# Kernel optimization log

Hardware: AMD Instinct MI355X
Metric: run time of the kernel (lower is better)

## Reference

```python
import jax, jax.numpy as jnp
import numpy as np

N_NODE = 40000
EMB = 100
LAYERS = 2
B = 512
L = 50
N = 50
E = 800000


def _l2norm(x, axis=-1, eps=1e-12):
    n = jnp.sqrt(jnp.sum(x * x, axis=axis, keepdims=True))
    return x / jnp.maximum(n, eps)


def _item_conv(rows, cols, vals, emb, b):
    # sparse A @ X repeated LAYERS times, stack, l2-normalize rows, weighted sum
    finals = [emb]
    x = emb
    for _ in range(LAYERS):
        x = jax.ops.segment_sum(vals[:, None] * x[cols], rows, num_segments=emb.shape[0])
        finals.append(x)
    f = _l2norm(jnp.stack(finals, 0))                      # [LAYERS+1, n, d]
    return jnp.sum(b[:, None, None] * f, axis=0)


def _session_conv(adj_dense, emb, a):
    finals = [emb]
    x = emb
    for _ in range(LAYERS):
        x = adj_dense @ x
        finals.append(x)
    f = _l2norm(jnp.stack(finals, 0))
    return jnp.sum(a[:, None, None] * f, axis=0)


def _gat(h, adj, a0, a1, a2, a3):
    # e_k[b,i,j] = leakyrelu(sum_d h[b,i,d]*h[b,j,d]*a_k[d]); never materialize [B,N,N,D]
    def score(a):
        return jax.nn.leaky_relu(jnp.einsum('bid,bjd->bij', h * a[:, 0], h), 0.2)
    e0, e1, e2, e3 = score(a0), score(a1), score(a2), score(a3)
    neg = jnp.float32(-9e15)
    alpha = jnp.where(adj == 1, e0, neg)
    alpha = jnp.where(adj == 2, e1, alpha)
    alpha = jnp.where(adj == 3, e2, alpha)
    alpha = jnp.where(adj == 4, e3, alpha)
    alpha = jax.nn.softmax(alpha, axis=-1)
    return jnp.einsum('bij,bjd->bid', alpha, h)


def _get_seq(emb_table, rev, h, alias, mix=0.8):
    seq_h = emb_table[rev]                                  # [B,L,D]
    bidx = jnp.arange(rev.shape[0])[:, None]
    seq_h_ = h[bidx, alias]                                 # [B,L,D]
    return (1.0 - mix) * seq_h + mix * seq_h_               # eval: dropout = identity


def _soft_attention(seq_h, mask_f, session_len, pos_emb, w1_W, w1_b, glu1_W, glu1_b, glu2_W, w2):
    hs = jnp.sum(seq_h, axis=1) / session_len               # [B,D]
    pos = jnp.broadcast_to(pos_emb[:seq_h.shape[1]][None], seq_h.shape)
    nh = jnp.tanh(jnp.concatenate([pos, seq_h], -1) @ w1_W.T + w1_b)
    nh = jax.nn.sigmoid(nh @ glu1_W.T + glu1_b + (hs @ glu2_W.T)[:, None, :])
    beta = (nh @ w2) * mask_f[..., None]                    # [B,L,1]
    return jnp.sum(beta * seq_h, axis=1)                    # [B,D]


def setup_inputs() -> dict:
    key = jax.random.key(0)
    ks = jax.random.split(key, 30)
    stdv = 1.0 / np.sqrt(EMB)
    u = lambda k, s: jax.random.uniform(k, s, jnp.float32, -stdv, stdv)
    return {
        'tar': jax.random.randint(ks[0], (B,), 0, N_NODE),
        'reversed_sess_item': jax.random.randint(ks[1], (B, L), 0, N_NODE + 1),
        'mask': jnp.ones((B, L), jnp.int32),
        'session_len': jnp.ones((B, 1), jnp.float32),
        'session_adj': jax.random.uniform(ks[2], (B, B), jnp.float32),
        'is_train': 0,
        'items': jax.random.randint(ks[3], (B, N), 0, N_NODE + 1),
        'adj': jax.random.randint(ks[4], (B, N, N), 0, 5),
        'alias_session': jax.random.randint(ks[5], (B, L), 0, N),
        'gnn_rows': jax.random.randint(ks[6], (E,), 0, N_NODE),
        'gnn_cols': jax.random.randint(ks[7], (E,), 0, N_NODE),
        'gnn_vals': jax.random.uniform(ks[8], (E,), jnp.float32),
        'nodes_emb': u(ks[9], (N_NODE, EMB)),
        'b_item': jnp.ones((LAYERS + 1,), jnp.float32),
        'a_sess': jnp.ones((LAYERS + 1,), jnp.float32),
        'a0': u(ks[10], (EMB, 1)), 'a1': u(ks[11], (EMB, 1)),
        'a2': u(ks[12], (EMB, 1)), 'a3': u(ks[13], (EMB, 1)),
        'w1_W': u(ks[14], (EMB, 2 * EMB)), 'w1_b': u(ks[15], (EMB,)),
        'w2': u(ks[16], (EMB, 1)),
        'glu1_W': u(ks[17], (EMB, EMB)), 'glu1_b': u(ks[18], (EMB,)),
        'glu2_W': u(ks[19], (EMB, EMB)),
        'pos_emb': u(ks[20], (150, EMB)),
    }


def reference(tar, reversed_sess_item, mask, session_len, session_adj, is_train,
              items, adj, alias_session, gnn_rows, gnn_cols, gnn_vals,
              nodes_emb, b_item, a_sess, a0, a1, a2, a3,
              w1_W, w1_b, w2, glu1_W, glu1_b, glu2_W, pos_emb):
    mask_f = mask.astype(jnp.float32)
    zeros = jnp.zeros((1, EMB), jnp.float32)
    emb_gnn = _item_conv(gnn_rows, gnn_cols, gnn_vals, nodes_emb, b_item)
    # eval mode: both dropouts are identity
    e1t = jnp.concatenate([zeros, emb_gnn], 0)
    e2t = jnp.concatenate([zeros, emb_gnn], 0)
    embeddings = e1t + e2t

    h1 = _gat(e1t[items], adj, a0, a1, a2, a3)
    h1 = _get_seq(e1t, reversed_sess_item, h1, alias_session, 0.8)
    h2 = _gat(e2t[items], adj, a0, a1, a2, a3)
    h2 = _get_seq(e2t, reversed_sess_item, h2, alias_session, 0.8)

    sel1 = _soft_attention(h1, mask_f, session_len, pos_emb, w1_W, w1_b, glu1_W, glu1_b, glu2_W, w2)
    sel1 = _session_conv(session_adj, sel1, a_sess)
    sel2 = _soft_attention(h2, mask_f, session_len, pos_emb, w1_W, w1_b, glu1_W, glu1_b, glu2_W, w2)
    sel2 = _session_conv(session_adj, sel2, a_sess)

    con_loss = jnp.float32(0.0)  # is_train == 0 (inference path)

    seq_h = sel1 + sel2
    scores = seq_h @ embeddings[1:].T                       # [B, N_NODE]
    logp = jax.nn.log_softmax(scores + 1e-8, axis=-1)
    loss = -jnp.mean(logp[jnp.arange(scores.shape[0]), tar])
    return (con_loss, loss, scores)
```

## Files before the change

kernel.cpp:

```cpp
#include <hip/hip_runtime.h>
#include <hip/hip_bf16.h>
#include <math.h>

#define N_NODE 40000
#define EMB 100
#define BB 512
#define LL 50
#define NI 50
#define EDG 800000
#define SCAN_BLOCKS 157

typedef short s16x8 __attribute__((ext_vector_type(8)));
typedef float f32x4 __attribute__((ext_vector_type(4)));

__global__ void khist(const int* __restrict__ rows, int* __restrict__ counts) {
  int e = blockIdx.x * 256 + threadIdx.x;
  atomicAdd(&counts[rows[e]], 1);
}

__global__ __launch_bounds__(256) void kscan1(const int* __restrict__ counts,
                                              int* __restrict__ scanout,
                                              int* __restrict__ blocksums, int n) {
  __shared__ int wsum[4];
  int tid = threadIdx.x;
  int i = blockIdx.x * 256 + tid;
  int v = (i < n) ? counts[i] : 0;
  int x = v;
  #pragma unroll
  for (int off = 1; off < 64; off <<= 1) {
    int t = __shfl_up(x, off, 64);
    if ((tid & 63) >= off) x += t;
  }
  int w = tid >> 6, lane = tid & 63;
  if (lane == 63) wsum[w] = x;
  __syncthreads();
  int woff = 0;
  #pragma unroll
  for (int k = 0; k < 4; ++k) woff += (k < w) ? wsum[k] : 0;
  int incl = x + woff;
  if (i < n) scanout[i] = incl - v;
  if (tid == 255) blocksums[blockIdx.x] = incl;
}

__global__ __launch_bounds__(256) void kscan2(int* __restrict__ blocksums, int nb) {
  __shared__ int wsum[4];
  int tid = threadIdx.x;
  int v = (tid < nb) ? blocksums[tid] : 0;
  int x = v;
  #pragma unroll
  for (int off = 1; off < 64; off <<= 1) {
    int t = __shfl_up(x, off, 64);
    if ((tid & 63) >= off) x += t;
  }
  int w = tid >> 6, lane = tid & 63;
  if (lane == 63) wsum[w] = x;
  __syncthreads();
  int woff = 0;
  #pragma unroll
  for (int k = 0; k < 4; ++k) woff += (k < w) ? wsum[k] : 0;
  if (tid < nb) blocksums[tid] = x + woff - v;
}

__global__ __launch_bounds__(256) void kscan3(const int* __restrict__ scanout,
                                              const int* __restrict__ blocksums,
                                              int* __restrict__ starts,
                                              int* __restrict__ cursor, int n) {
  int i = blockIdx.x * 256 + threadIdx.x;
  if (i < n) {
    int s = scanout[i] + blocksums[blockIdx.x];
    starts[i] = s;
    cursor[i] = s;
  }
}

__global__ void kfill(const int* __restrict__ rows, const int* __restrict__ cols,
                      const float* __restrict__ vals, int* __restrict__ cursor,
                      int* __restrict__ colS, float* __restrict__ valS) {
  int e = blockIdx.x * 256 + threadIdx.x;
  int r = rows[e];
  int p = atomicAdd(&cursor[r], 1);
  colS[p] = cols[e];
  valS[p] = vals[e];
}

__global__ __launch_bounds__(256) void kspmm(const int* __restrict__ starts,
                                             const int* __restrict__ counts,
                                             const int* __restrict__ colS,
                                             const float* __restrict__ valS,
                                             const float* __restrict__ x,
                                             float* __restrict__ out) {
  int row = blockIdx.x * 4 + (threadIdx.x >> 6);
  int lane = threadIdx.x & 63;
  int s = starts[row], cnt = counts[row];
  bool act = lane < 50;
  int d2 = (act ? lane : 49) * 2;
  float ax = 0.f, ay = 0.f;
  for (int base = 0; base < cnt; base += 64) {
    int nb = cnt - base; if (nb > 64) nb = 64;
    int cl = 0; float vl = 0.f;
    if (lane < nb) {
      cl = colS[s + base + lane];
      vl = valS[s + base + lane];
    }
    int t = 0;
    for (; t + 4 <= nb; t += 4) {
      int c0 = __shfl(cl, t),     c1 = __shfl(cl, t + 1);
      int c2 = __shfl(cl, t + 2), c3 = __shfl(cl, t + 3);
      float v0 = __shfl(vl, t),     v1 = __shfl(vl, t + 1);
      float v2 = __shfl(vl, t + 2), v3 = __shfl(vl, t + 3);
      float2 g0 = *(const float2*)(x + (size_t)c0 * EMB + d2);
      float2 g1 = *(const float2*)(x + (size_t)c1 * EMB + d2);
      float2 g2 = *(const float2*)(x + (size_t)c2 * EMB + d2);
      float2 g3 = *(const float2*)(x + (size_t)c3 * EMB + d2);
      ax += v0 * g0.x; ay += v0 * g0.y;
      ax += v1 * g1.x; ay += v1 * g1.y;
      ax += v2 * g2.x; ay += v2 * g2.y;
      ax += v3 * g3.x; ay += v3 * g3.y;
    }
    for (; t < nb; ++t) {
      int c = __shfl(cl, t);
      float v = __shfl(vl, t);
      float2 g = *(const float2*)(x + (size_t)c * EMB + d2);
      ax += v * g.x; ay += v * g.y;
    }
  }
  if (act) {
    float2 o; o.x = ax; o.y = ay;
    *(float2*)(out + (size_t)row * EMB + d2) = o;
  }
}

__global__ void kcomb(const float* __restrict__ x0, const float* __restrict__ x1,
                      const float* __restrict__ x2, const float* __restrict__ bI,
                      float* __restrict__ emb) {
  int n = blockIdx.x * 4 + (threadIdx.x >> 6);
  int lane = threadIdx.x & 63;
  int d0 = lane, d1 = lane + 64;
  bool h1 = d1 < EMB;
  size_t base = (size_t)n * EMB;
  float v00 = x0[base + d0], v01 = h1 ? x0[base + d1] : 0.f;
  float v10 = x1[base + d0], v11 = h1 ? x1[base + d1] : 0.f;
  float v20 = x2[base + d0], v21 = h1 ? x2[base + d1] : 0.f;
  float q0 = v00 * v00 + v01 * v01;
  float q1 = v10 * v10 + v11 * v11;
  float q2 = v20 * v20 + v21 * v21;
  #pragma unroll
  for (int off = 32; off; off >>= 1) {
    q0 += __shfl_xor(q0, off);
    q1 += __shfl_xor(q1, off);
    q2 += __shfl_xor(q2, off);
  }
  float r0 = 1.f / fmaxf(sqrtf(q0), 1e-12f);
  float r1 = 1.f / fmaxf(sqrtf(q1), 1e-12f);
  float r2 = 1.f / fmaxf(sqrtf(q2), 1e-12f);
  float b0 = bI[0], b1 = bI[1], b2 = bI[2];
  emb[base + d0] = b0 * v00 * r0 + b1 * v10 * r1 + b2 * v20 * r2;
  if (h1) emb[base + d1] = b0 * v01 * r0 + b1 * v11 * r1 + b2 * v21 * r2;
}

__global__ __launch_bounds__(256) void kgat(
    const float* __restrict__ emb, const int* __restrict__ items,
    const int* __restrict__ adj,
    const float* __restrict__ a0p, const float* __restrict__ a1p,
    const float* __restrict__ a2p, const float* __restrict__ a3p,
    float* __restrict__ hgat) {
  __shared__ __align__(16) float hl[64 * 108];
  __shared__ __align__(16) float as[4 * 100];
  __shared__ float al[4][4][64];
  int b = blockIdx.x, half = blockIdx.y;
  int tid = threadIdx.x;
  for (int idx = tid; idx < 400; idx += 256) {
    int k = idx / 100, d = idx % 100;
    const float* ap = (k == 0) ? a0p : (k == 1) ? a1p : (k == 2) ? a2p : a3p;
    as[idx] = ap[d];
  }
  for (int idx = tid; idx < 64 * 50; idx += 256) {
    int i = idx / 50, d2 = (idx % 50) * 2;
    float2 v; v.x = 0.f; v.y = 0.f;
    if (i < NI) {
      int node = items[b * NI + i];
      if (node != 0) v = *(const float2*)(emb + (size_t)(node - 1) * EMB + d2);
    }
    *(float2*)&hl[i * 108 + d2] = v;
  }
  __syncthreads();
  int w = tid >> 6, lane = tid & 63;
  int i0 = half * 25 + w * 7;
  int nIw = 25 - w * 7; if (nIw > 7) nIw = 7;
  const float* hjrow = &hl[lane * 108];
  int u2 = lane >> 5, dq = lane & 31;
  int dqc = (dq < 25) ? dq : 24;
  for (int g = 0; g < nIw; g += 4) {
    int ib = i0 + g;
    int rem = nIw - g;
    int ir[4], av[4];
    const float* asel[4];
    #pragma unroll
    for (int u = 0; u < 4; ++u) {
      int i = ib + u; ir[u] = (i < NI) ? i : NI - 1;
      av[u] = (lane < NI) ? adj[(size_t)b * (NI * NI) + ir[u] * NI + lane] : 0;
      int k = av[u] - 1; if (k < 0) k = 0; if (k > 3) k = 3;
      asel[u] = &as[k * 100];
    }
    float acc[4];
    #pragma unroll
    for (int u = 0; u < 4; ++u) acc[u] = 0.f;
    for (int d0 = 0; d0 < 100; d0 += 4) {
      float4 hj = *(const float4*)(hjrow + d0);
      #pragma unroll
      for (int u = 0; u < 4; ++u) {
        float4 hi = *(const float4*)&hl[ir[u] * 108 + d0];
        float4 aw = *(const float4*)(asel[u] + d0);
        float p0 = hi.x * hj.x, p1 = hi.y * hj.y;
        float p2 = hi.z * hj.z, p3 = hi.w * hj.w;
        acc[u] += p0 * aw.x + p1 * aw.y + p2 * aw.z + p3 * aw.w;
      }
    }
    #pragma unroll
    for (int u = 0; u < 4; ++u) {
      float sv = acc[u];
      sv = (sv >= 0.f) ? sv : 0.2f * sv;
      float e = (av[u] == 0) ? -9e15f : sv;
      if (lane >= NI) e = -INFINITY;
      float m = e;
      #pragma unroll
      for (int off = 32; off; off >>= 1) m = fmaxf(m, __shfl_xor(m, off));
      float p = expf(e - m);
      float s = p;
      #pragma unroll
      for (int off = 32; off; off >>= 1) s += __shfl_xor(s, off);
      al[w][u][lane] = p / s;
    }
    #pragma unroll
    for (int pass = 0; pass < 2; ++pass) {
      int u = pass * 2 + u2;
      int i = ib + u;
      const float* alr = al[w][u];
      float ox = 0.f, oy = 0.f, oz = 0.f, ow = 0.f;
      for (int j = 0; j < NI; ++j) {
        float a = alr[j];
        float4 hv = *(const float4*)&hl[j * 108 + dqc * 4];
        ox += a * hv.x; oy += a * hv.y; oz += a * hv.z; ow += a * hv.w;
      }
      if (dq < 25 && u < rem) {
        float4 o4; o4.x = ox; o4.y = oy; o4.z = oz; o4.w = ow;
        *(float4*)&hgat[((size_t)b * NI + i) * EMB + dq * 4] = o4;
      }
    }
  }
}

__global__ void kseq(const float* __restrict__ emb, const int* __restrict__ rev,
                     const int* __restrict__ alias, const float* __restrict__ hgat,
                     float* __restrict__ hseq) {
  int idx = blockIdx.x * 256 + threadIdx.x;
  int b = idx / 5000, r = idx % 5000, l = r / 100, d = r % 100;
  int node = rev[b * LL + l];
  float sh = (node == 0) ? 0.f : emb[(size_t)(node - 1) * EMB + d];
  int a = alias[b * LL + l];
  float shh = hgat[((size_t)b * NI + a) * EMB + d];
  hseq[idx] = 0.2f * sh + 0.8f * shh;
}

__global__ void kprep_t(const float* __restrict__ w1W, const float* __restrict__ g1W,
                        const float* __restrict__ g2W, float* __restrict__ w1t2,
                        float* __restrict__ g1t, float* __restrict__ g2t) {
  int idx = blockIdx.x * 256 + threadIdx.x;
  if (idx >= 10000) return;
  int c = idx / 100, o = idx % 100;
  w1t2[c * 100 + o] = w1W[o * 200 + 100 + c];
  g1t[c * 100 + o] = g1W[o * 100 + c];
  g2t[c * 100 + o] = g2W[o * 100 + c];
}

__global__ void kprep_pos(const float* __restrict__ posE, const float* __restrict__ w1W,
                          const float* __restrict__ w1b, float* __restrict__ posW) {
  int idx = blockIdx.x * 256 + threadIdx.x;
  if (idx >= 5000) return;
  int l = idx / 100, o = idx % 100;
  float acc = w1b[o];
  for (int c = 0; c < 100; ++c) acc += posE[l * 100 + c] * w1W[o * 200 + c];
  posW[idx] = acc;
}

__global__ __launch_bounds__(256) void ksoft(
    const float* __restrict__ hseqG, const float* __restrict__ slenp,
    const int* __restrict__ maskp,
    const float* __restrict__ posW, const float* __restrict__ w1t2,
    const float* __restrict__ glu1t, const float* __restrict__ glu1b,
    const float* __restrict__ glu2t, const float* __restrict__ w2,
    float* __restrict__ sel) {
  __shared__ float hq[LL * 101];
  __shared__ float nh[LL * 100];
  __shared__ float red[25 * 52];
  __shared__ float hs_s[100];
  __shared__ float g_s[100];
  __shared__ float beta_s[LL];
  int b = blockIdx.x, tid = threadIdx.x;
  for (int idx = tid; idx < LL * 100; idx += 256) {
    int l = idx / 100, d = idx % 100;
    hq[l * 101 + d] = hseqG[((size_t)b * LL + l) * 100 + d];
  }
  __syncthreads();
  if (tid < 100) {
    float s = 0.f;
    for (int l = 0; l < LL; ++l) s += hq[l * 101 + tid];
    hs_s[tid] = s / slenp[b];
  }
  __syncthreads();
  if (tid < 100) {
    float acc = 0.f;
    for (int c = 0; c < 100; ++c) acc += hs_s[c] * glu2t[c * 100 + tid];
    g_s[tid] = acc;
  }
  int lg = tid / 25, og = tid % 25;
  if (tid < 250) {
    float acc[5][4];
    #pragma unroll
    for (int j = 0; j < 5; ++j) {
      float4 p = *(const float4*)&posW[(lg * 5 + j) * 100 + og * 4];
      acc[j][0] = p.x; acc[j][1] = p.y; acc[j][2] = p.z; acc[j][3] = p.w;
    }
    for (int c = 0; c < 100; ++c) {
      float4 wv = *(const float4*)&w1t2[c * 100 + og * 4];
      float hv[5];
      #pragma unroll
      for (int j = 0; j < 5; ++j) hv[j] = hq[(lg * 5 + j) * 101 + c];
      #pragma unroll
      for (int j = 0; j < 5; ++j) {
        acc[j][0] += hv[j] * wv.x;
        acc[j][1] += hv[j] * wv.y;
        acc[j][2] += hv[j] * wv.z;
        acc[j][3] += hv[j] * wv.w;
      }
    }
    #pragma unroll
    for (int j = 0; j < 5; ++j) {
      float4 t;
      t.x = tanhf(acc[j][0]); t.y = tanhf(acc[j][1]);
      t.z = tanhf(acc[j][2]); t.w = tanhf(acc[j][3]);
      *(float4*)&nh[(lg * 5 + j) * 100 + og * 4] = t;
    }
  }
  __syncthreads();
  if (tid < 250) {
    float4 gb = *(const float4*)&glu1b[og * 4];
    float4 gg = *(const float4*)&g_s[og * 4];
    float base0 = gg.x + gb.x, base1 = gg.y + gb.y, base2 = gg.z + gb.z, base3 = gg.w + gb.w;
    float acc[5][4];
    #pragma unroll
    for (int j = 0; j < 5; ++j) {
      acc[j][0] = base0; acc[j][1] = base1; acc[j][2] = base2; acc[j][3] = base3;
    }
    for (int c = 0; c < 100; ++c) {
      float4 wv = *(const float4*)&glu1t[c * 100 + og * 4];
      float hv[5];
      #pragma unroll
      for (int j = 0; j < 5; ++j) hv[j] = nh[(lg * 5 + j) * 100 + c];
      #pragma unroll
      for (int j = 0; j < 5; ++j) {
        acc[j][0] += hv[j] * wv.x;
        acc[j][1] += hv[j] * wv.y;
        acc[j][2] += hv[j] * wv.z;
        acc[j][3] += hv[j] * wv.w;
      }
    }
    float4 w2v = *(const float4*)&w2[og * 4];
    #pragma unroll
    for (int j = 0; j < 5; ++j) {
      float s0 = w2v.x / (1.f + expf(-acc[j][0]));
      float s1 = w2v.y / (1.f + expf(-acc[j][1]));
      float s2 = w2v.z / (1.f + expf(-acc[j][2]));
      float s3 = w2v.w / (1.f + expf(-acc[j][3]));
      red[og * 52 + lg * 5 + j] = (s0 + s1) + (s2 + s3);
    }
  }
  __syncthreads();
  if (tid < LL) {
    float s = 0.f;
    for (int og2 = 0; og2 < 25; ++og2) s += red[og2 * 52 + tid];
    beta_s[tid] = s * (float)maskp[b * LL + tid];
  }
  __syncthreads();
  if (tid < 100) {
    float acc = 0.f;
    for (int l = 0; l < LL; ++l) acc += beta_s[l] * hq[l * 101 + tid];
    sel[(size_t)b * 100 + tid] = acc;
  }
}

__global__ void ksess(const float* __restrict__ adjS, const float* __restrict__ x,
                      float* __restrict__ out) {
  int b = blockIdx.x, d = threadIdx.x;
  if (d >= 100) return;
  const float* ar = adjS + (size_t)b * BB;
  float a0 = 0.f, a1 = 0.f, a2 = 0.f, a3 = 0.f;
  for (int j = 0; j < BB; j += 4) {
    a0 += ar[j]     * x[(j)     * 100 + d];
    a1 += ar[j + 1] * x[(j + 1) * 100 + d];
    a2 += ar[j + 2] * x[(j + 2) * 100 + d];
    a3 += ar[j + 3] * x[(j + 3) * 100 + d];
  }
  out[(size_t)b * 100 + d] = (a0 + a1) + (a2 + a3);
}

__global__ void ksesscomb(const float* __restrict__ x0, const float* __restrict__ x1,
                          const float* __restrict__ x2, const float* __restrict__ aS,
                          float* __restrict__ out) {
  int b = blockIdx.x * 4 + (threadIdx.x >> 6);
  int lane = threadIdx.x & 63;
  int d0 = lane, d1 = lane + 64;
  bool h1 = d1 < EMB;
  size_t base = (size_t)b * EMB;
  float v00 = x0[base + d0], v01 = h1 ? x0[base + d1] : 0.f;
  float v10 = x1[base + d0], v11 = h1 ? x1[base + d1] : 0.f;
  float v20 = x2[base + d0], v21 = h1 ? x2[base + d1] : 0.f;
  float q0 = v00 * v00 + v01 * v01;
  float q1 = v10 * v10 + v11 * v11;
  float q2 = v20 * v20 + v21 * v21;
  #pragma unroll
  for (int off = 32; off; off >>= 1) {
    q0 += __shfl_xor(q0, off);
    q1 += __shfl_xor(q1, off);
    q2 += __shfl_xor(q2, off);
  }
  float r0 = 1.f / fmaxf(sqrtf(q0), 1e-12f);
  float r1 = 1.f / fmaxf(sqrtf(q1), 1e-12f);
  float r2 = 1.f / fmaxf(sqrtf(q2), 1e-12f);
  float b0 = aS[0], b1 = aS[1], b2 = aS[2];
  out[base + d0] = 2.f * (b0 * v00 * r0 + b1 * v10 * r1 + b2 * v20 * r2);
  if (h1) out[base + d1] = 2.f * (b0 * v01 * r0 + b1 * v11 * r1 + b2 * v21 * r2);
}

__global__ void kprepB(const float* __restrict__ emb, unsigned short* __restrict__ bHi,
                       unsigned short* __restrict__ bLo) {
  int idx = blockIdx.x * 256 + threadIdx.x;
  int n = idx >> 7, k = idx & 127;
  float v = (k < EMB) ? 2.f * emb[(size_t)n * EMB + k] : 0.f;
  __hip_bfloat16 h = __float2bfloat16(v);
  float rem = v - __bfloat162float(h);
  __hip_bfloat16 l = __float2bfloat16(rem);
  bHi[idx] = *reinterpret_cast<unsigned short*>(&h);
  bLo[idx] = *reinterpret_cast<unsigned short*>(&l);
}

__global__ void kprepA(const float* __restrict__ seqh, unsigned short* __restrict__ aHi,
                       unsigned short* __restrict__ aLo) {
  int idx = blockIdx.x * 256 + threadIdx.x;
  int n = idx >> 7, k = idx & 127;
  float v = (k < EMB) ? seqh[(size_t)n * EMB + k] : 0.f;
  __hip_bfloat16 h = __float2bfloat16(v);
  float rem = v - __bfloat162float(h);
  __hip_bfloat16 l = __float2bfloat16(rem);
  aHi[idx] = *reinterpret_cast<unsigned short*>(&h);
  aLo[idx] = *reinterpret_cast<unsigned short*>(&l);
}

__global__ __launch_bounds__(256) void kscoresM(
    const unsigned short* __restrict__ aHi, const unsigned short* __restrict__ aLo,
    const unsigned short* __restrict__ bHi, const unsigned short* __restrict__ bLo,
    float* __restrict__ outS) {
  __shared__ __align__(16) unsigned short Bh[64 * 136];
  __shared__ __align__(16) unsigned short Bl[64 * 136];
  int tid = threadIdx.x;
  int n0 = blockIdx.x * 64, b0 = blockIdx.y * 64;
  int w = tid >> 6, lane = tid & 63;
  int ln = lane & 15, quad = lane >> 4;

  const unsigned short* aRowH = aHi + (size_t)(b0 + w * 16 + ln) * 128 + quad * 8;
  const unsigned short* aRowL = aLo + (size_t)(b0 + w * 16 + ln) * 128 + quad * 8;
  s16x8 ah[4], al[4];
  #pragma unroll
  for (int s = 0; s < 4; ++s) {
    ah[s] = *(const s16x8*)(aRowH + s * 32);
    al[s] = *(const s16x8*)(aRowL + s * 32);
  }

  #pragma unroll
  for (int it = 0; it < 4; ++it) {
    int seg = tid + it * 256;
    int r = seg >> 4, q = seg & 15;
    *(s16x8*)&Bh[r * 136 + q * 8] = *(const s16x8*)&bHi[(size_t)(n0 + r) * 128 + q * 8];
    *(s16x8*)&Bl[r * 136 + q * 8] = *(const s16x8*)&bLo[(size_t)(n0 + r) * 128 + q * 8];
  }
  __syncthreads();

  f32x4 acc[4];
  #pragma unroll
  for (int t = 0; t < 4; ++t) acc[t] = (f32x4){0.f, 0.f, 0.f, 0.f};

  #pragma unroll
  for (int s = 0; s < 4; ++s) {
    #pragma unroll
    for (int t = 0; t < 4; ++t) {
      s16x8 bh = *(const s16x8*)&Bh[(t * 16 + ln) * 136 + s * 32 + quad * 8];
      s16x8 bl = *(const s16x8*)&Bl[(t * 16 + ln) * 136 + s * 32 + quad * 8];
      acc[t] = __builtin_amdgcn_mfma_f32_16x16x32_bf16(ah[s], bh, acc[t], 0, 0, 0);
      acc[t] = __builtin_amdgcn_mfma_f32_16x16x32_bf16(al[s], bh, acc[t], 0, 0, 0);
      acc[t] = __builtin_amdgcn_mfma_f32_16x16x32_bf16(ah[s], bl, acc[t], 0, 0, 0);
    }
  }

  int brow = b0 + w * 16 + quad * 4;
  #pragma unroll
  for (int t = 0; t < 4; ++t) {
    int ncol = n0 + t * 16 + ln;
    #pragma unroll
    for (int r = 0; r < 4; ++r) {
      outS[(size_t)(brow + r) * N_NODE + ncol] = acc[t][r];
    }
  }
}

__global__ __launch_bounds__(256) void klse(const float* __restrict__ outS,
                                            const int* __restrict__ tar,
                                            float* __restrict__ part) {
  __shared__ float ms[256], ss[256];
  int b = blockIdx.x, tid = threadIdx.x;
  const float2* sp = (const float2*)(outS + (size_t)b * N_NODE);
  float m = -INFINITY, s = 0.f;
  for (int i = tid; i < N_NODE / 2; i += 256) {
    float2 v = sp[i];
    float mx = fmaxf(v.x, v.y);
    float add = expf(v.x - mx) + expf(v.y - mx);
    if (mx > m) { s = s * expf(m - mx) + add; m = mx; }
    else s += add * expf(mx - m);
  }
  ms[tid] = m; ss[tid] = s;
  __syncthreads();
  for (int st = 128; st; st >>= 1) {
    if (tid < st) {
      float m2 = ms[tid + st], s2 = ss[tid + st];
      float M = fmaxf(ms[tid], m2);
      ss[tid] = ss[tid] * expf(ms[tid] - M) + s2 * expf(m2 - M);
      ms[tid] = M;
    }
    __syncthreads();
  }
  if (tid == 0) {
    float tsc = outS[(size_t)b * N_NODE + tar[b]];
    part[b] = tsc - (ms[0] + logf(ss[0]));
  }
}

__global__ void kfinal(const float* __restrict__ part, float* __restrict__ out) {
  __shared__ float red[256];
  int tid = threadIdx.x;
  red[tid] = part[tid] + part[tid + 256];
  __syncthreads();
  for (int st = 128; st; st >>= 1) {
    if (tid < st) red[tid] += red[tid + st];
    __syncthreads();
  }
  if (tid == 0) {
    out[0] = 0.f;
    out[1] = -red[0] / (float)BB;
  }
}

extern "C" void kernel_launch(void* const* d_in, const int* in_sizes, int n_in,
                              void* d_out, int out_size, void* d_ws, size_t ws_size,
                              hipStream_t stream) {
  const int* tar    = (const int*)d_in[0];
  const int* rev    = (const int*)d_in[1];
  const int* maskp  = (const int*)d_in[2];
  const float* slen = (const float*)d_in[3];
  const float* sadj = (const float*)d_in[4];
  const int* items  = (const int*)d_in[6];
  const int* adjp   = (const int*)d_in[7];
  const int* alias  = (const int*)d_in[8];
  const int* grows  = (const int*)d_in[9];
  const int* gcols  = (const int*)d_in[10];
  const float* gvals = (const float*)d_in[11];
  const float* nemb = (const float*)d_in[12];
  const float* bI   = (const float*)d_in[13];
  const float* aS   = (const float*)d_in[14];
  const float* a0p  = (const float*)d_in[15];
  const float* a1p  = (const float*)d_in[16];
  const float* a2p  = (const float*)d_in[17];
  const float* a3p  = (const float*)d_in[18];
  const float* w1W  = (const float*)d_in[19];
  const float* w1b  = (const float*)d_in[20];
  const float* w2p  = (const float*)d_in[21];
  const float* g1W  = (const float*)d_in[22];
  const float* g1b  = (const float*)d_in[23];
  const float* g2W  = (const float*)d_in[24];
  const float* posE = (const float*)d_in[25];

  float* W = (float*)d_ws;
  size_t o = 0;
  float* emb_gnn = W + o; o += (size_t)N_NODE * EMB;
  float* x1      = W + o; o += (size_t)N_NODE * EMB;
  float* x2      = W + o; o += (size_t)N_NODE * EMB;
  float* sel     = W + o; o += (size_t)BB * EMB;
  float* y1      = W + o; o += (size_t)BB * EMB;
  float* y2      = W + o; o += (size_t)BB * EMB;
  float* seqh    = W + o; o += (size_t)BB * EMB;
  float* posW    = W + o; o += 5120;
  float* w1t2    = W + o; o += 10000;
  float* glu1t   = W + o; o += 10000;
  float* glu2t   = W + o; o += 10000;
  float* valS    = W + o; o += EDG;
  float* part    = W + o; o += 512;
  int* colS   = (int*)(W + o); o += EDG;
  int* counts = (int*)(W + o); o += N_NODE;
  int* starts = (int*)(W + o); o += N_NODE;
  int* cursor = (int*)(W + o); o += N_NODE;
  int* scantmp = (int*)(W + o); o += N_NODE;
  int* blocksums = (int*)(W + o); o += 256;
  unsigned short* aHi = (unsigned short*)(W + o); o += 32768;
  unsigned short* aLo = (unsigned short*)(W + o); o += 32768;
  float* hgat = x1;
  float* hseq = x2;
  unsigned short* bHi = (unsigned short*)x1;
  unsigned short* bLo = (unsigned short*)x2;

  float* outF = (float*)d_out;
  float* outScores = outF + 2;

  hipMemsetAsync(counts, 0, N_NODE * sizeof(int), stream);
  khist<<<EDG / 256, 256, 0, stream>>>(grows, counts);
  kscan1<<<SCAN_BLOCKS, 256, 0, stream>>>(counts, scantmp, blocksums, N_NODE);
  kscan2<<<1, 256, 0, stream>>>(blocksums, SCAN_BLOCKS);
  kscan3<<<SCAN_BLOCKS, 256, 0, stream>>>(scantmp, blocksums, starts, cursor, N_NODE);
  kfill<<<EDG / 256, 256, 0, stream>>>(grows, gcols, gvals, cursor, colS, valS);
  kspmm<<<N_NODE / 4, 256, 0, stream>>>(starts, counts, colS, valS, nemb, x1);
  kspmm<<<N_NODE / 4, 256, 0, stream>>>(starts, counts, colS, valS, x1, x2);
  kcomb<<<N_NODE / 4, 256, 0, stream>>>(nemb, x1, x2, bI, emb_gnn);
  kgat<<<dim3(BB, 2), 256, 0, stream>>>(emb_gnn, items, adjp, a0p, a1p, a2p, a3p, hgat);
  kseq<<<(BB * LL * EMB) / 256, 256, 0, stream>>>(emb_gnn, rev, alias, hgat, hseq);
  kprep_t<<<40, 256, 0, stream>>>(w1W, g1W, g2W, w1t2, glu1t, glu2t);
  kprep_pos<<<20, 256, 0, stream>>>(posE, w1W, w1b, posW);
  ksoft<<<BB, 256, 0, stream>>>(hseq, slen, maskp, posW, w1t2, glu1t, g1b, glu2t, w2p, sel);
  kprepB<<<(N_NODE * 128) / 256, 256, 0, stream>>>(emb_gnn, bHi, bLo);
  ksess<<<BB, 128, 0, stream>>>(sadj, sel, y1);
  ksess<<<BB, 128, 0, stream>>>(sadj, y1, y2);
  ksesscomb<<<BB / 4, 256, 0, stream>>>(sel, y1, y2, aS, seqh);
  kprepA<<<(BB * 128) / 256, 256, 0, stream>>>(seqh, aHi, aLo);
  kscoresM<<<dim3(N_NODE / 64, BB / 64), 256, 0, stream>>>(aHi, aLo, bHi, bLo, outScores);
  klse<<<BB, 256, 0, stream>>>(outScores, tar, part);
  kfinal<<<1, 256, 0, stream>>>(part, outF);
}
```

Measured before the change: 566.3 us.

## Restructure GAT kernel to one block per session with register-held rows

The GAT kernel now runs one block per session instead of two. Each lane holds its node's embedding row in registers, and the four waves split the neighbour index j into chunks of 13. The softmax max and sum are combined across waves through shared memory, and alpha is written to LDS so the weighted sum can be split by feature quads across waves. The SpMM gather also gains an 8-way unrolled loop to put more loads in flight. The aim is to stop recomputing and re-reading data between the two half-blocks and to raise reuse of the per-row data. The costs are heavy register pressure (25 float4 plus 13 scores per lane), extra block-wide syncs and half as many blocks.

```diff
diff --git a/kernel.cpp b/kernel.cpp
--- a/kernel.cpp
+++ b/kernel.cpp
@@ -103,6 +103,32 @@
       vl = valS[s + base + lane];
     }
     int t = 0;
+    for (; t + 8 <= nb; t += 8) {
+      int c0 = __shfl(cl, t),     c1 = __shfl(cl, t + 1);
+      int c2 = __shfl(cl, t + 2), c3 = __shfl(cl, t + 3);
+      int c4 = __shfl(cl, t + 4), c5 = __shfl(cl, t + 5);
+      int c6 = __shfl(cl, t + 6), c7 = __shfl(cl, t + 7);
+      float v0 = __shfl(vl, t),     v1 = __shfl(vl, t + 1);
+      float v2 = __shfl(vl, t + 2), v3 = __shfl(vl, t + 3);
+      float v4 = __shfl(vl, t + 4), v5 = __shfl(vl, t + 5);
+      float v6 = __shfl(vl, t + 6), v7 = __shfl(vl, t + 7);
+      float2 g0 = *(const float2*)(x + (size_t)c0 * EMB + d2);
+      float2 g1 = *(const float2*)(x + (size_t)c1 * EMB + d2);
+      float2 g2 = *(const float2*)(x + (size_t)c2 * EMB + d2);
+      float2 g3 = *(const float2*)(x + (size_t)c3 * EMB + d2);
+      float2 g4 = *(const float2*)(x + (size_t)c4 * EMB + d2);
+      float2 g5 = *(const float2*)(x + (size_t)c5 * EMB + d2);
+      float2 g6 = *(const float2*)(x + (size_t)c6 * EMB + d2);
+      float2 g7 = *(const float2*)(x + (size_t)c7 * EMB + d2);
+      ax += v0 * g0.x; ay += v0 * g0.y;
+      ax += v1 * g1.x; ay += v1 * g1.y;
+      ax += v2 * g2.x; ay += v2 * g2.y;
+      ax += v3 * g3.x; ay += v3 * g3.y;
+      ax += v4 * g4.x; ay += v4 * g4.y;
+      ax += v5 * g5.x; ay += v5 * g5.y;
+      ax += v6 * g6.x; ay += v6 * g6.y;
+      ax += v7 * g7.x; ay += v7 * g7.y;
+    }
     for (; t + 4 <= nb; t += 4) {
       int c0 = __shfl(cl, t),     c1 = __shfl(cl, t + 1);
       int c2 = __shfl(cl, t + 2), c3 = __shfl(cl, t + 3);
@@ -166,8 +192,9 @@
     float* __restrict__ hgat) {
   __shared__ __align__(16) float hl[64 * 108];
   __shared__ __align__(16) float as[4 * 100];
-  __shared__ float al[4][4][64];
-  int b = blockIdx.x, half = blockIdx.y;
+  __shared__ float alpha_lds[64 * 51];
+  __shared__ float wred[4][2][64];
+  int b = blockIdx.x;
   int tid = threadIdx.x;
   for (int idx = tid; idx < 400; idx += 256) {
     int k = idx / 100, d = idx % 100;
@@ -185,66 +212,88 @@
   }
   __syncthreads();
   int w = tid >> 6, lane = tid & 63;
-  int i0 = half * 25 + w * 7;
-  int nIw = 25 - w * 7; if (nIw > 7) nIw = 7;
-  const float* hjrow = &hl[lane * 108];
-  int u2 = lane >> 5, dq = lane & 31;
-  int dqc = (dq < 25) ? dq : 24;
-  for (int g = 0; g < nIw; g += 4) {
-    int ib = i0 + g;
-    int rem = nIw - g;
-    int ir[4], av[4];
-    const float* asel[4];
-    #pragma unroll
-    for (int u = 0; u < 4; ++u) {
-      int i = ib + u; ir[u] = (i < NI) ? i : NI - 1;
-      av[u] = (lane < NI) ? adj[(size_t)b * (NI * NI) + ir[u] * NI + lane] : 0;
-      int k = av[u] - 1; if (k < 0) k = 0; if (k > 3) k = 3;
-      asel[u] = &as[k * 100];
-    }
-    float acc[4];
-    #pragma unroll
-    for (int u = 0; u < 4; ++u) acc[u] = 0.f;
-    for (int d0 = 0; d0 < 100; d0 += 4) {
-      float4 hj = *(const float4*)(hjrow + d0);
+  int j0 = w * 13;
+  int nj = 50 - j0; if (nj > 13) nj = 13;
+
+  float4 hreg[25];
+  #pragma unroll
+  for (int q = 0; q < 25; ++q) hreg[q] = *(const float4*)&hl[lane * 108 + q * 4];
+
+  int al_lane = (lane < NI) ? lane : NI - 1;
+  const int* adjrow = adj + (size_t)b * (NI * NI) + al_lane * NI + j0;
+  int adjv[13];
+  #pragma unroll
+  for (int t = 0; t < 13; ++t) adjv[t] = (t < nj) ? adjrow[t] : 0;
+
+  float e[13];
+  #pragma unroll
+  for (int jj = 0; jj < 13; ++jj) {
+    float acc = 0.f;
+    if (jj < nj) {
+      int j = j0 + jj;
+      int k = adjv[jj] - 1; k = (k < 0) ? 0 : (k > 3) ? 3 : k;
+      const float* aw = &as[k * 100];
       #pragma unroll
-      for (int u = 0; u < 4; ++u) {
-        float4 hi = *(const float4*)&hl[ir[u] * 108 + d0];
-        float4 aw = *(const float4*)(asel[u] + d0);
-        float p0 = hi.x * hj.x, p1 = hi.y * hj.y;
-        float p2 = hi.z * hj.z, p3 = hi.w * hj.w;
-        acc[u] += p0 * aw.x + p1 * aw.y + p2 * aw.z + p3 * aw.w;
+      for (int q = 0; q < 25; ++q) {
+        float4 hj = *(const float4*)&hl[j * 108 + q * 4];
+        float4 a4 = *(const float4*)(aw + q * 4);
+        float4 hm = hreg[q];
+        acc += hm.x * hj.x * a4.x + hm.y * hj.y * a4.y
+             + hm.z * hj.z * a4.z + hm.w * hj.w * a4.w;
       }
-    }
-    #pragma unroll
-    for (int u = 0; u < 4; ++u) {
-      float sv = acc[u];
-      sv = (sv >= 0.f) ? sv : 0.2f * sv;
-      float e = (av[u] == 0) ? -9e15f : sv;
-      if (lane >= NI) e = -INFINITY;
-      float m = e;
-      #pragma unroll
-      for (int off = 32; off; off >>= 1) m = fmaxf(m, __shfl_xor(m, off));
-      float p = expf(e - m);
-      float s = p;
-      #pragma unroll
-      for (int off = 32; off; off >>= 1) s += __shfl_xor(s, off);
-      al[w][u][lane] = p / s;
-    }
-    #pragma unroll
-    for (int pass = 0; pass < 2; ++pass) {
-      int u = pass * 2 + u2;
-      int i = ib + u;
-      const float* alr = al[w][u];
-      float ox = 0.f, oy = 0.f, oz = 0.f, ow = 0.f;
-      for (int j = 0; j < NI; ++j) {
-        float a = alr[j];
-        float4 hv = *(const float4*)&hl[j * 108 + dqc * 4];
-        ox += a * hv.x; oy += a * hv.y; oz += a * hv.z; ow += a * hv.w;
+      acc = (acc >= 0.f) ? acc : 0.2f * acc;
+      acc = (adjv[jj] == 0) ? -9e15f : acc;
+    } else {
+      acc = -INFINITY;
+    }
+    e[jj] = acc;
+  }
+
+  float mloc = -INFINITY;
+  #pragma unroll
+  for (int jj = 0; jj < 13; ++jj) if (jj < nj) mloc = fmaxf(mloc, e[jj]);
+  wred[w][0][lane] = mloc;
+  __syncthreads();
+  float m = fmaxf(fmaxf(wred[0][0][lane], wred[1][0][lane]),
+                  fmaxf(wred[2][0][lane], wred[3][0][lane]));
+  float sloc = 0.f;
+  #pragma unroll
+  for (int jj = 0; jj < 13; ++jj) if (jj < nj) {
+    e[jj] = expf(e[jj] - m);
+    sloc += e[jj];
+  }
+  wred[w][1][lane] = sloc;
+  __syncthreads();
+  float s = (wred[0][1][lane] + wred[1][1][lane]) +
+            (wred[2][1][lane] + wred[3][1][lane]);
+  float inv = 1.f / s;
+  #pragma unroll
+  for (int jj = 0; jj < 13; ++jj) if (jj < nj)
+    alpha_lds[lane * 51 + j0 + jj] = e[jj] * inv;
+  __syncthreads();
+
+  int nq = (w == 0) ? 7 : 6;
+  float4 outq[7];
+  #pragma unroll
+  for (int t = 0; t < 7; ++t) outq[t] = make_float4(0.f, 0.f, 0.f, 0.f);
+  for (int j = 0; j < NI; ++j) {
+    float aj = alpha_lds[lane * 51 + j];
+    #pragma unroll
+    for (int t = 0; t < 7; ++t) {
+      if (t < nq) {
+        int q = w + 4 * t;
+        float4 hv = *(const float4*)&hl[j * 108 + q * 4];
+        outq[t].x += aj * hv.x; outq[t].y += aj * hv.y;
+        outq[t].z += aj * hv.z; outq[t].w += aj * hv.w;
       }
-      if (dq < 25 && u < rem) {
-        float4 o4; o4.x = ox; o4.y = oy; o4.z = oz; o4.w = ow;
-        *(float4*)&hgat[((size_t)b * NI + i) * EMB + dq * 4] = o4;
+    }
+  }
+  if (lane < NI) {
+    #pragma unroll
+    for (int t = 0; t < 7; ++t) {
+      if (t < nq) {
+        int q = w + 4 * t;
+        *(float4*)&hgat[((size_t)b * NI + lane) * EMB + q * 4] = outq[t];
       }
     }
   }
@@ -627,7 +676,7 @@
   kspmm<<<N_NODE / 4, 256, 0, stream>>>(starts, counts, colS, valS, nemb, x1);
   kspmm<<<N_NODE / 4, 256, 0, stream>>>(starts, counts, colS, valS, x1, x2);
   kcomb<<<N_NODE / 4, 256, 0, stream>>>(nemb, x1, x2, bI, emb_gnn);
-  kgat<<<dim3(BB, 2), 256, 0, stream>>>(emb_gnn, items, adjp, a0p, a1p, a2p, a3p, hgat);
+  kgat<<<BB, 256, 0, stream>>>(emb_gnn, items, adjp, a0p, a1p, a2p, a3p, hgat);
   kseq<<<(BB * LL * EMB) / 256, 256, 0, stream>>>(emb_gnn, rev, alias, hgat, hseq);
   kprep_t<<<40, 256, 0, stream>>>(w1W, g1W, g2W, w1t2, glu1t, glu2t);
   kprep_pos<<<20, 256, 0, stream>>>(posE, w1W, w1b, posW);
```

Measured after the change: 544.3 us. 1.04x faster.
